# Kernel optimization log

Measured on AMD Instinct MI355X. Metric: run time of the kernel, lower is better.

Reference implementation:

```python
import jax, jax.numpy as jnp
import numpy as np

N = 50000
E = 800000
IN_C, HID_C, OUT_C = 128, 128, 40
K = 3  # PyG TAGConv default number of hops


def setup_inputs() -> dict:
    key = jax.random.key(0)
    k1, k2, k3, k4, k5, k6, k7 = jax.random.split(key, 7)
    x = jax.random.normal(k1, (N, IN_C), dtype=jnp.float32)
    edge_index = jax.random.randint(k2, (2, E), 0, N, dtype=jnp.int64)
    # Linear((K+1)*in, out) weights (stored as [in_total, out] for x @ W)
    s1 = 1.0 / np.sqrt((K + 1) * IN_C)
    s2 = 1.0 / np.sqrt((K + 1) * HID_C)
    W1 = jax.random.uniform(k3, ((K + 1) * IN_C, HID_C), jnp.float32, -s1, s1)
    b1 = jax.random.uniform(k4, (HID_C,), jnp.float32, -s1, s1)
    W2 = jax.random.uniform(k5, ((K + 1) * HID_C, OUT_C), jnp.float32, -s2, s2)
    b2 = jax.random.uniform(k6, (OUT_C,), jnp.float32, -s2, s2)
    return {"x": x, "edge_index": edge_index, "W1": W1, "b1": b1, "W2": W2, "b2": b2}


def _sym_norm(src, dst):
    # GCN-style symmetric normalization: deg computed on destination (col)
    deg = jax.ops.segment_sum(jnp.ones((E,), jnp.float32), dst, num_segments=N)
    dis = jnp.where(deg > 0, jax.lax.rsqrt(jnp.maximum(deg, 1.0)), 0.0)
    return dis[src] * dis[dst]  # [E]


def _tag_layer(x, src, dst, norm, W, b):
    xs = [x]
    h = x
    for _ in range(K):
        h = jax.ops.segment_sum(h[src] * norm[:, None], dst, num_segments=N)
        xs.append(h)
    return jnp.concatenate(xs, axis=1) @ W + b


def reference(x, edge_index, W1, b1, W2, b2):
    src, dst = edge_index[0], edge_index[1]
    norm = _sym_norm(src, dst)
    h = jax.nn.relu(_tag_layer(x, src, dst, norm, W1, b1))
    # F.dropout(training=False) is identity at inference
    h = _tag_layer(h, src, dst, norm, W2, b2)
    return jax.nn.log_softmax(h, axis=1)
```

## Files before the change

### kernel.cpp

```cpp
#include <hip/hip_runtime.h>
#include <hip/hip_bf16.h>

#define NNODES 50000
#define NROWP  50176
#define NEDGES 800000
#define KHOP 3
#define NBKT 196
#define BCAP 6144
#define ABLK 800
#define ACH  1000

typedef __attribute__((ext_vector_type(8))) short short8v;
typedef __attribute__((ext_vector_type(8))) __bf16 bf16x8;
typedef __attribute__((ext_vector_type(4))) float f32x4;

__device__ inline unsigned short f2bf(float f) {
  unsigned u = __builtin_bit_cast(unsigned, f);
  u += 0x7fffu + ((u >> 16) & 1u);
  return (unsigned short)(u >> 16);
}
__device__ inline float bflo(unsigned u) { return __builtin_bit_cast(float, u << 16); }
__device__ inline float bfhi(unsigned u) { return __builtin_bit_cast(float, u & 0xffff0000u); }

__device__ inline void gload_lds16(const void* g, void* l) {
  __builtin_amdgcn_global_load_lds(
      (const __attribute__((address_space(1))) unsigned int*)g,
      (__attribute__((address_space(3))) unsigned int*)l, 16, 0, 0);
}

__device__ inline f32x4 mfma_bf16(bf16x8 a, bf16x8 b, f32x4 c) {
  return __builtin_amdgcn_mfma_f32_16x16x32_bf16(a, b, c, 0, 0, 0);
}

__device__ inline void fma8(float* acc, float w, short8v v) {
  uint4 u = __builtin_bit_cast(uint4, v);
  acc[0] = fmaf(w, bflo(u.x), acc[0]);
  acc[1] = fmaf(w, bfhi(u.x), acc[1]);
  acc[2] = fmaf(w, bflo(u.y), acc[2]);
  acc[3] = fmaf(w, bfhi(u.y), acc[3]);
  acc[4] = fmaf(w, bflo(u.z), acc[4]);
  acc[5] = fmaf(w, bfhi(u.z), acc[5]);
  acc[6] = fmaf(w, bflo(u.w), acc[6]);
  acc[7] = fmaf(w, bfhi(u.w), acc[7]);
}

__device__ inline void fma4(float* acc, float w, uint2 v) {
  acc[0] = fmaf(w, bflo(v.x), acc[0]);
  acc[1] = fmaf(w, bfhi(v.x), acc[1]);
  acc[2] = fmaf(w, bflo(v.y), acc[2]);
  acc[3] = fmaf(w, bfhi(v.y), acc[3]);
}

__global__ __launch_bounds__(256) void bucketA_kernel(
    const int* __restrict__ src, const int* __restrict__ dst,
    int* __restrict__ bcur, int2* __restrict__ bkt) {
  __shared__ int2 eb[ACH];
  __shared__ int hist[256];
  __shared__ int base[256];
  int tid = threadIdx.x;
  int e0 = blockIdx.x * ACH;
  int cnt = NEDGES - e0; if (cnt > ACH) cnt = ACH;
  hist[tid] = 0;
  __syncthreads();
  for (int i = tid; i < cnt; i += 256) {
    int s = src[e0 + i], d = dst[e0 + i];
    eb[i] = make_int2(s, d);
    atomicAdd(&hist[d >> 8], 1);
  }
  __syncthreads();
  base[tid] = atomicAdd(&bcur[tid], hist[tid]);
  hist[tid] = 0;
  __syncthreads();
  for (int i = tid; i < cnt; i += 256) {
    int2 e = eb[i];
    int b = e.y >> 8;
    int off = atomicAdd(&hist[b], 1);
    bkt[(size_t)b * BCAP + base[b] + off] = e;
  }
}

__global__ __launch_bounds__(256) void bktscan_kernel(
    const int* __restrict__ bcur, int* __restrict__ boff, int* __restrict__ row_ptr) {
  __shared__ int sd[256];
  int tid = threadIdx.x;
  int own = (tid < NBKT) ? bcur[tid] : 0;
  sd[tid] = own;
  __syncthreads();
  for (int o = 1; o < 256; o <<= 1) {
    int t = (tid >= o) ? sd[tid - o] : 0;
    __syncthreads();
    sd[tid] += t;
    __syncthreads();
  }
  if (tid < NBKT) boff[tid] = sd[tid] - own;
  if (tid == 255) row_ptr[NNODES] = sd[255];
}

__global__ __launch_bounds__(256) void histC_kernel(
    const int* __restrict__ bcur, const int2* __restrict__ bkt,
    const int* __restrict__ boff, int* __restrict__ row_ptr,
    float* __restrict__ dis, int n) {
  __shared__ int h[256];
  __shared__ int sc[256];
  int b = blockIdx.x, tid = threadIdx.x;
  h[tid] = 0;
  __syncthreads();
  int sz = bcur[b];
  for (int i = tid; i < sz; i += 256)
    atomicAdd(&h[bkt[(size_t)b * BCAP + i].y & 255], 1);
  __syncthreads();
  int own = h[tid];
  sc[tid] = own;
  __syncthreads();
  for (int o = 1; o < 256; o <<= 1) {
    int t = (tid >= o) ? sc[tid - o] : 0;
    __syncthreads();
    sc[tid] += t;
    __syncthreads();
  }
  int node = b * 256 + tid;
  if (node < n) {
    row_ptr[node] = boff[b] + sc[tid] - own;
    dis[node] = (own > 0) ? rsqrtf((float)own) : 0.f;
  }
}

__global__ __launch_bounds__(256) void scatB_kernel(
    const int* __restrict__ bcur, const int2* __restrict__ bkt,
    const int* __restrict__ row_ptr, const float* __restrict__ dis,
    int2* __restrict__ csr, int n) {
  __shared__ int cur[256];
  int b = blockIdx.x, tid = threadIdx.x;
  int node = b * 256 + tid;
  cur[tid] = (node < n) ? row_ptr[node] : 0;
  __syncthreads();
  int sz = bcur[b];
  for (int i = tid; i < sz; i += 256) {
    int2 e = bkt[(size_t)b * BCAP + i];
    int pos = atomicAdd(&cur[e.y & 255], 1);
    int2 ent;
    ent.x = e.x;
    ent.y = __float_as_int(dis[e.x] * dis[e.y]);
    csr[pos] = ent;
  }
}

__global__ void wprep_kernel(const float* __restrict__ W1, const float* __restrict__ W2,
                             unsigned short* __restrict__ W1t,
                             unsigned short* __restrict__ W2pt) {
  int t = blockIdx.x * blockDim.x + threadIdx.x;
  if (t < 512 * 128) {
    int c = t >> 9, k = t & 511;
    W1t[t] = f2bf(W1[(size_t)k * 128 + c]);
  } else if (t < 512 * 128 + 160 * 128) {
    int u = t - 512 * 128;
    int q = u >> 7, r = u & 127;
    int k = q / 40, c = q - k * 40;
    W2pt[u] = f2bf(W2[(size_t)(k * 128 + r) * 40 + c]);
  }
}

__global__ void copyx_kernel(const float* __restrict__ x, unsigned short* __restrict__ P, int n) {
  int t = blockIdx.x * blockDim.x + threadIdx.x;
  int i = t >> 5;
  int c4 = (t & 31) << 2;
  if (i < n) {
    float4 v = *(const float4*)&x[(size_t)i * 128 + c4];
    unsigned lo = (unsigned)f2bf(v.x) | ((unsigned)f2bf(v.y) << 16);
    unsigned hi = (unsigned)f2bf(v.z) | ((unsigned)f2bf(v.w) << 16);
    uint2 o; o.x = lo; o.y = hi;
    *(uint2*)&P[(size_t)i * 512 + c4] = o;
  }
}

__global__ __launch_bounds__(256) void prop128c_kernel(
    const unsigned short* __restrict__ in, unsigned short* __restrict__ out,
    const int* __restrict__ row_ptr, const int2* __restrict__ csr, int n) {
  int node = (int)((blockIdx.x * blockDim.x + threadIdx.x) >> 6);
  int lane = threadIdx.x & 63;
  if (node >= n) return;
  int beg = row_ptr[node], end = row_ptr[node + 1];
  int deg = end - beg;
  int2 ent = make_int2(0, 0);
  if (lane < deg) ent = csr[beg + lane];
  const int grp = lane >> 4, sub = lane & 15;
  float acc[8] = {0.f, 0.f, 0.f, 0.f, 0.f, 0.f, 0.f, 0.f};
  int m = deg < 64 ? deg : 64;
  int j = 0;
  for (; j + 16 <= m; j += 16) {
    int s0 = __shfl(ent.x, j + grp, 64);
    float w0 = __int_as_float(__shfl(ent.y, j + grp, 64));
    int s1 = __shfl(ent.x, j + 4 + grp, 64);
    float w1 = __int_as_float(__shfl(ent.y, j + 4 + grp, 64));
    int s2 = __shfl(ent.x, j + 8 + grp, 64);
    float w2 = __int_as_float(__shfl(ent.y, j + 8 + grp, 64));
    int s3 = __shfl(ent.x, j + 12 + grp, 64);
    float w3 = __int_as_float(__shfl(ent.y, j + 12 + grp, 64));
    short8v v0 = *(const short8v*)(in + (size_t)s0 * 512 + sub * 8);
    short8v v1 = *(const short8v*)(in + (size_t)s1 * 512 + sub * 8);
    short8v v2 = *(const short8v*)(in + (size_t)s2 * 512 + sub * 8);
    short8v v3 = *(const short8v*)(in + (size_t)s3 * 512 + sub * 8);
    fma8(acc, w0, v0);
    fma8(acc, w1, v1);
    fma8(acc, w2, v2);
    fma8(acc, w3, v3);
  }
  for (; j + 8 <= m; j += 8) {
    int s0 = __shfl(ent.x, j + grp, 64);
    float w0 = __int_as_float(__shfl(ent.y, j + grp, 64));
    int s1 = __shfl(ent.x, j + 4 + grp, 64);
    float w1 = __int_as_float(__shfl(ent.y, j + 4 + grp, 64));
    short8v v0 = *(const short8v*)(in + (size_t)s0 * 512 + sub * 8);
    short8v v1 = *(const short8v*)(in + (size_t)s1 * 512 + sub * 8);
    fma8(acc, w0, v0);
    fma8(acc, w1, v1);
  }
  for (; j < m; j += 4) {
    int idx = j + grp;
    bool act = idx < m;
    int ic = act ? idx : m - 1;
    int s0 = __shfl(ent.x, ic, 64);
    float w0 = __int_as_float(__shfl(ent.y, ic, 64));
    if (!act) w0 = 0.f;
    short8v v0 = *(const short8v*)(in + (size_t)s0 * 512 + sub * 8);
    fma8(acc, w0, v0);
  }
  for (int t = beg + 64; t < end; ++t) {
    int2 e0 = csr[t];
    float w0 = (grp == 0) ? __int_as_float(e0.y) : 0.f;
    short8v v = *(const short8v*)(in + (size_t)e0.x * 512 + sub * 8);
    fma8(acc, w0, v);
  }
#pragma unroll
  for (int i = 0; i < 8; ++i) {
    acc[i] += __shfl_xor(acc[i], 16, 64);
    acc[i] += __shfl_xor(acc[i], 32, 64);
  }
  if (grp == 0) {
    uint4 r;
    r.x = (unsigned)f2bf(acc[0]) | ((unsigned)f2bf(acc[1]) << 16);
    r.y = (unsigned)f2bf(acc[2]) | ((unsigned)f2bf(acc[3]) << 16);
    r.z = (unsigned)f2bf(acc[4]) | ((unsigned)f2bf(acc[5]) << 16);
    r.w = (unsigned)f2bf(acc[6]) | ((unsigned)f2bf(acc[7]) << 16);
    *(uint4*)(out + (size_t)node * 512 + sub * 8) = r;
  }
}

__global__ __launch_bounds__(256) void gemm12_kernel(
    const unsigned short* __restrict__ A,
    const unsigned short* __restrict__ B1t,
    const float* __restrict__ bias,
    const unsigned short* __restrict__ B2t,
    unsigned short* __restrict__ G) {
  __shared__ short smem[2048 + 4096 + 64 * 136];
  short* As  = smem;
  short* Bs1 = smem + 2048;
  short* Ht  = smem + 2048 + 4096;
  short* Bs2c = smem;
  const int tid = threadIdx.x;
  const int lane = tid & 63;
  const int w = tid >> 6;
  const int wr = w & 1;
  const int wc = w >> 1;
  const int row0 = blockIdx.x * 64;
  const int lrow = lane >> 2;
  const int lkp = lane & 3;
  const int kg = lane >> 4, rr = lane & 15;

  f32x4 acc[2][4];
#pragma unroll
  for (int i = 0; i < 2; ++i)
#pragma unroll
    for (int j = 0; j < 4; ++j) acc[i][j] = (f32x4)0.f;

  for (int k0 = 0; k0 < 512; k0 += 32) {
    gload_lds16(A + (size_t)(row0 + w * 16 + lrow) * 512 + k0 + lkp * 8, &As[w * 512]);
    gload_lds16(B1t + (size_t)(w * 16 + lrow) * 512 + k0 + lkp * 8, &Bs1[w * 512]);
    gload_lds16(B1t + (size_t)((w + 4) * 16 + lrow) * 512 + k0 + lkp * 8, &Bs1[(w + 4) * 512]);
    __syncthreads();
    bf16x8 af[2], bfr[4];
#pragma unroll
    for (int mr = 0; mr < 2; ++mr)
      af[mr] = __builtin_bit_cast(bf16x8,
          *(const short8v*)&As[(wr * 32 + mr * 16 + rr) * 32 + kg * 8]);
#pragma unroll
    for (int nr = 0; nr < 4; ++nr)
      bfr[nr] = __builtin_bit_cast(bf16x8,
          *(const short8v*)&Bs1[(wc * 64 + nr * 16 + rr) * 32 + kg * 8]);
#pragma unroll
    for (int mr = 0; mr < 2; ++mr)
#pragma unroll
      for (int nr = 0; nr < 4; ++nr)
        acc[mr][nr] = mfma_bf16(af[mr], bfr[nr], acc[mr][nr]);
    __syncthreads();
  }
  {
    const int cg = lane >> 4, cl = lane & 15;
#pragma unroll
    for (int mr = 0; mr < 2; ++mr)
#pragma unroll
      for (int nr = 0; nr < 4; ++nr) {
        int col = wc * 64 + nr * 16 + cl;
        float bv = bias[col];
#pragma unroll
        for (int j = 0; j < 4; ++j) {
          int lr = wr * 32 + mr * 16 + cg * 4 + j;
          Ht[lr * 136 + col] = (short)f2bf(fmaxf(acc[mr][nr][j] + bv, 0.f));
        }
      }
  }
  __syncthreads();

  f32x4 acc2[10];
#pragma unroll
  for (int i = 0; i < 10; ++i) acc2[i] = (f32x4)0.f;

  for (int k0 = 0; k0 < 128; k0 += 32) {
    for (int c = w; c < 10; c += 4)
      gload_lds16(B2t + (size_t)(c * 16 + lrow) * 128 + k0 + lkp * 8, &Bs2c[c * 512]);
    __syncthreads();
    bf16x8 af = __builtin_bit_cast(bf16x8,
        *(const short8v*)&Ht[(w * 16 + rr) * 136 + k0 + kg * 8]);
#pragma unroll
    for (int nr = 0; nr < 10; ++nr) {
      bf16x8 bfr = __builtin_bit_cast(bf16x8,
          *(const short8v*)&Bs2c[(nr * 16 + rr) * 32 + kg * 8]);
      acc2[nr] = mfma_bf16(af, bfr, acc2[nr]);
    }
    __syncthreads();
  }
  {
    const int cg = lane >> 4, cl = lane & 15;
#pragma unroll
    for (int nr = 0; nr < 10; ++nr) {
      int col = nr * 16 + cl;
      int k = col / 40;
      int o = col - k * 40;
#pragma unroll
      for (int j = 0; j < 4; ++j) {
        int row = row0 + w * 16 + cg * 4 + j;
        G[(size_t)k * NROWP * 64 + (size_t)row * 64 + o] = f2bf(acc2[nr][j]);
      }
    }
  }
}

__global__ __launch_bounds__(256) void prop40c_kernel(
    const unsigned short* __restrict__ in,
    const unsigned short* __restrict__ add,
    unsigned short* __restrict__ out,
    const int* __restrict__ row_ptr, const int2* __restrict__ csr, int n) {
  int node = (int)((blockIdx.x * blockDim.x + threadIdx.x) >> 6);
  int lane = threadIdx.x & 63;
  if (node >= n) return;
  int beg = row_ptr[node], end = row_ptr[node + 1];
  int deg = end - beg;
  int2 ent = make_int2(0, 0);
  if (lane < deg) ent = csr[beg + lane];
  const int grp = lane >> 4, sub = lane & 15;
  float acc[4] = {0.f, 0.f, 0.f, 0.f};
  if (grp == 0) {
    uint2 a = *(const uint2*)(add + (size_t)node * 64 + sub * 4);
    acc[0] = bflo(a.x); acc[1] = bfhi(a.x);
    acc[2] = bflo(a.y); acc[3] = bfhi(a.y);
  }
  int m = deg < 64 ? deg : 64;
  int j = 0;
  for (; j + 16 <= m; j += 16) {
    int s0 = __shfl(ent.x, j + grp, 64);
    float w0 = __int_as_float(__shfl(ent.y, j + grp, 64));
    int s1 = __shfl(ent.x, j + 4 + grp, 64);
    float w1 = __int_as_float(__shfl(ent.y, j + 4 + grp, 64));
    int s2 = __shfl(ent.x, j + 8 + grp, 64);
    float w2 = __int_as_float(__shfl(ent.y, j + 8 + grp, 64));
    int s3 = __shfl(ent.x, j + 12 + grp, 64);
    float w3 = __int_as_float(__shfl(ent.y, j + 12 + grp, 64));
    uint2 v0 = *(const uint2*)(in + (size_t)s0 * 64 + sub * 4);
    uint2 v1 = *(const uint2*)(in + (size_t)s1 * 64 + sub * 4);
    uint2 v2 = *(const uint2*)(in + (size_t)s2 * 64 + sub * 4);
    uint2 v3 = *(const uint2*)(in + (size_t)s3 * 64 + sub * 4);
    fma4(acc, w0, v0);
    fma4(acc, w1, v1);
    fma4(acc, w2, v2);
    fma4(acc, w3, v3);
  }
  for (; j + 8 <= m; j += 8) {
    int s0 = __shfl(ent.x, j + grp, 64);
    float w0 = __int_as_float(__shfl(ent.y, j + grp, 64));
    int s1 = __shfl(ent.x, j + 4 + grp, 64);
    float w1 = __int_as_float(__shfl(ent.y, j + 4 + grp, 64));
    uint2 v0 = *(const uint2*)(in + (size_t)s0 * 64 + sub * 4);
    uint2 v1 = *(const uint2*)(in + (size_t)s1 * 64 + sub * 4);
    fma4(acc, w0, v0);
    fma4(acc, w1, v1);
  }
  for (; j < m; j += 4) {
    int idx = j + grp;
    bool act = idx < m;
    int ic = act ? idx : m - 1;
    int s0 = __shfl(ent.x, ic, 64);
    float w0 = __int_as_float(__shfl(ent.y, ic, 64));
    if (!act) w0 = 0.f;
    uint2 v0 = *(const uint2*)(in + (size_t)s0 * 64 + sub * 4);
    fma4(acc, w0, v0);
  }
  for (int t = beg + 64; t < end; ++t) {
    int2 e0 = csr[t];
    float w = (grp == 0) ? __int_as_float(e0.y) : 0.f;
    uint2 v = *(const uint2*)(in + (size_t)e0.x * 64 + sub * 4);
    fma4(acc, w, v);
  }
#pragma unroll
  for (int i = 0; i < 4; ++i) {
    acc[i] += __shfl_xor(acc[i], 16, 64);
    acc[i] += __shfl_xor(acc[i], 32, 64);
  }
  if (grp == 0) {
    uint2 r;
    r.x = (unsigned)f2bf(acc[0]) | ((unsigned)f2bf(acc[1]) << 16);
    r.y = (unsigned)f2bf(acc[2]) | ((unsigned)f2bf(acc[3]) << 16);
    *(uint2*)(out + (size_t)node * 64 + sub * 4) = r;
  }
}

__global__ __launch_bounds__(256) void prop40c_lsm_kernel(
    const unsigned short* __restrict__ in,
    const unsigned short* __restrict__ add,
    const float* __restrict__ b2,
    float* __restrict__ out,
    const int* __restrict__ row_ptr, const int2* __restrict__ csr, int n) {
  int node = (int)((blockIdx.x * blockDim.x + threadIdx.x) >> 6);
  int lane = threadIdx.x & 63;
  if (node >= n) return;
  int beg = row_ptr[node], end = row_ptr[node + 1];
  int deg = end - beg;
  int2 ent = make_int2(0, 0);
  if (lane < deg) ent = csr[beg + lane];
  const int grp = lane >> 4, sub = lane & 15;
  float acc[4] = {0.f, 0.f, 0.f, 0.f};
  if (grp == 0) {
    uint2 a = *(const uint2*)(add + (size_t)node * 64 + sub * 4);
    acc[0] = bflo(a.x); acc[1] = bfhi(a.x);
    acc[2] = bflo(a.y); acc[3] = bfhi(a.y);
  }
  int m = deg < 64 ? deg : 64;
  int j = 0;
  for (; j + 16 <= m; j += 16) {
    int s0 = __shfl(ent.x, j + grp, 64);
    float w0 = __int_as_float(__shfl(ent.y, j + grp, 64));
    int s1 = __shfl(ent.x, j + 4 + grp, 64);
    float w1 = __int_as_float(__shfl(ent.y, j + 4 + grp, 64));
    int s2 = __shfl(ent.x, j + 8 + grp, 64);
    float w2 = __int_as_float(__shfl(ent.y, j + 8 + grp, 64));
    int s3 = __shfl(ent.x, j + 12 + grp, 64);
    float w3 = __int_as_float(__shfl(ent.y, j + 12 + grp, 64));
    uint2 v0 = *(const uint2*)(in + (size_t)s0 * 64 + sub * 4);
    uint2 v1 = *(const uint2*)(in + (size_t)s1 * 64 + sub * 4);
    uint2 v2 = *(const uint2*)(in + (size_t)s2 * 64 + sub * 4);
    uint2 v3 = *(const uint2*)(in + (size_t)s3 * 64 + sub * 4);
    fma4(acc, w0, v0);
    fma4(acc, w1, v1);
    fma4(acc, w2, v2);
    fma4(acc, w3, v3);
  }
  for (; j + 8 <= m; j += 8) {
    int s0 = __shfl(ent.x, j + grp, 64);
    float w0 = __int_as_float(__shfl(ent.y, j + grp, 64));
    int s1 = __shfl(ent.x, j + 4 + grp, 64);
    float w1 = __int_as_float(__shfl(ent.y, j + 4 + grp, 64));
    uint2 v0 = *(const uint2*)(in + (size_t)s0 * 64 + sub * 4);
    uint2 v1 = *(const uint2*)(in + (size_t)s1 * 64 + sub * 4);
    fma4(acc, w0, v0);
    fma4(acc, w1, v1);
  }
  for (; j < m; j += 4) {
    int idx = j + grp;
    bool act = idx < m;
    int ic = act ? idx : m - 1;
    int s0 = __shfl(ent.x, ic, 64);
    float w0 = __int_as_float(__shfl(ent.y, ic, 64));
    if (!act) w0 = 0.f;
    uint2 v0 = *(const uint2*)(in + (size_t)s0 * 64 + sub * 4);
    fma4(acc, w0, v0);
  }
  for (int t = beg + 64; t < end; ++t) {
    int2 e0 = csr[t];
    float w = (grp == 0) ? __int_as_float(e0.y) : 0.f;
    uint2 v = *(const uint2*)(in + (size_t)e0.x * 64 + sub * 4);
    fma4(acc, w, v);
  }
#pragma unroll
  for (int i = 0; i < 4; ++i) {
    acc[i] += __shfl_xor(acc[i], 16, 64);
    acc[i] += __shfl_xor(acc[i], 32, 64);
  }
  bool val = (sub < 10);
  float vv[4];
  if (val) {
    float4 bv = *(const float4*)(b2 + sub * 4);
    vv[0] = acc[0] + bv.x; vv[1] = acc[1] + bv.y;
    vv[2] = acc[2] + bv.z; vv[3] = acc[3] + bv.w;
  } else {
    vv[0] = vv[1] = vv[2] = vv[3] = -__builtin_inff();
  }
  float mx = fmaxf(fmaxf(vv[0], vv[1]), fmaxf(vv[2], vv[3]));
#pragma unroll
  for (int o = 1; o < 16; o <<= 1) mx = fmaxf(mx, __shfl_xor(mx, o, 64));
  float s = 0.f;
  if (val)
    s = expf(vv[0] - mx) + expf(vv[1] - mx) + expf(vv[2] - mx) + expf(vv[3] - mx);
#pragma unroll
  for (int o = 1; o < 16; o <<= 1) s += __shfl_xor(s, o, 64);
  if (grp == 0 && val) {
    float ls = logf(s);
    float4 o4;
    o4.x = vv[0] - mx - ls; o4.y = vv[1] - mx - ls;
    o4.z = vv[2] - mx - ls; o4.w = vv[3] - mx - ls;
    *(float4*)(out + (size_t)node * 40 + sub * 4) = o4;
  }
}

extern "C" void kernel_launch(void* const* d_in, const int* in_sizes, int n_in,
                              void* d_out, int out_size, void* d_ws, size_t ws_size,
                              hipStream_t stream) {
  const float* x  = (const float*)d_in[0];
  const int*   ei = (const int*)d_in[1];
  const float* W1 = (const float*)d_in[2];
  const float* b1 = (const float*)d_in[3];
  const float* W2 = (const float*)d_in[4];
  const float* b2 = (const float*)d_in[5];
  const int* srcv = ei;
  const int* dstv = ei + NEDGES;
  float* out = (float*)d_out;

  char* wsb = (char*)d_ws;
  size_t off = 0;
  auto alloc = [&](size_t bytes) {
    char* p = wsb + off;
    off += (bytes + 255) & ~(size_t)255;
    return p;
  };
  float*          dis     = (float*)          alloc((size_t)NNODES * 4);
  int*            row_ptr = (int*)            alloc(((size_t)NNODES + 1) * 4);
  int*            bcur    = (int*)            alloc((size_t)256 * 4);
  int*            boff    = (int*)            alloc((size_t)NBKT * 4);
  int2*           bkt     = (int2*)           alloc((size_t)NBKT * BCAP * 8);
  int2*           csr     = (int2*)           alloc((size_t)NEDGES * 8);
  unsigned short* W1t     = (unsigned short*) alloc((size_t)128 * 512 * 2);
  unsigned short* W2pt    = (unsigned short*) alloc((size_t)160 * 128 * 2);
  unsigned short* P       = (unsigned short*) alloc((size_t)NROWP * 512 * 2);
  unsigned short* G       = (unsigned short*) alloc((size_t)4 * NROWP * 64 * 2);
  unsigned short* tb      = (unsigned short*) alloc((size_t)NNODES * 64 * 2);
  unsigned short* t2      = (unsigned short*) alloc((size_t)NNODES * 64 * 2);

  unsigned short* G0 = G;
  unsigned short* G1 = G + (size_t)1 * NROWP * 64;
  unsigned short* G2 = G + (size_t)2 * NROWP * 64;
  unsigned short* G3 = G + (size_t)3 * NROWP * 64;

  hipMemsetAsync(bcur, 0, 256 * 4, stream);
  bucketA_kernel<<<ABLK, 256, 0, stream>>>(srcv, dstv, bcur, bkt);
  bktscan_kernel<<<1, 256, 0, stream>>>(bcur, boff, row_ptr);
  histC_kernel<<<NBKT, 256, 0, stream>>>(bcur, bkt, boff, row_ptr, dis, NNODES);
  scatB_kernel<<<NBKT, 256, 0, stream>>>(bcur, bkt, row_ptr, dis, csr, NNODES);
  wprep_kernel<<<(512 * 128 + 160 * 128 + 255) / 256, 256, 0, stream>>>(W1, W2, W1t, W2pt);
  copyx_kernel<<<((NNODES * 32) + 255) / 256, 256, 0, stream>>>(x, P, NNODES);

  const int prop_blocks = (NNODES * 64 + 255) / 256;
  for (int k = 1; k <= KHOP; ++k)
    prop128c_kernel<<<prop_blocks, 256, 0, stream>>>(P + 128 * (k - 1), P + 128 * k,
                                                     row_ptr, csr, NNODES);
  const int gemm_blocks = (NNODES + 63) / 64;
  gemm12_kernel<<<gemm_blocks, 256, 0, stream>>>(P, W1t, b1, W2pt, G);
  prop40c_kernel<<<prop_blocks, 256, 0, stream>>>(G3, G2, tb, row_ptr, csr, NNODES);
  prop40c_kernel<<<prop_blocks, 256, 0, stream>>>(tb, G1, t2, row_ptr, csr, NNODES);
  prop40c_lsm_kernel<<<prop_blocks, 256, 0, stream>>>(t2, G0, b2, out, row_ptr, csr, NNODES);
}
```

Measured before the change: 229.6 us.

## Merge scan into histC, fuse prep kernels, widen prop40 to 8-lane groups

Folds the single-block bucket scan into every histC block, which recomputes the prefix redundantly, and merges the x-to-bf16 copy with the weight prep into one kernel, cutting the launch count. The 40-wide propagation kernels now have each lane load 16 bytes (8 bf16) instead of 8. Each row is then covered by 8 lanes rather than 16, so 8 edges are processed per step instead of 4. This trades more registers and shuffle-reduction steps for fewer, wider memory transactions.

```diff
diff --git a/kernel.cpp b/kernel.cpp
--- a/kernel.cpp
+++ b/kernel.cpp
@@ -44,13 +44,6 @@
   acc[7] = fmaf(w, bfhi(u.w), acc[7]);
 }
 
-__device__ inline void fma4(float* acc, float w, uint2 v) {
-  acc[0] = fmaf(w, bflo(v.x), acc[0]);
-  acc[1] = fmaf(w, bfhi(v.x), acc[1]);
-  acc[2] = fmaf(w, bflo(v.y), acc[2]);
-  acc[3] = fmaf(w, bfhi(v.y), acc[3]);
-}
-
 __global__ __launch_bounds__(256) void bucketA_kernel(
     const int* __restrict__ src, const int* __restrict__ dst,
     int* __restrict__ bcur, int2* __restrict__ bkt) {
@@ -79,32 +72,23 @@
   }
 }
 
-__global__ __launch_bounds__(256) void bktscan_kernel(
-    const int* __restrict__ bcur, int* __restrict__ boff, int* __restrict__ row_ptr) {
-  __shared__ int sd[256];
-  int tid = threadIdx.x;
-  int own = (tid < NBKT) ? bcur[tid] : 0;
-  sd[tid] = own;
-  __syncthreads();
-  for (int o = 1; o < 256; o <<= 1) {
-    int t = (tid >= o) ? sd[tid - o] : 0;
-    __syncthreads();
-    sd[tid] += t;
-    __syncthreads();
-  }
-  if (tid < NBKT) boff[tid] = sd[tid] - own;
-  if (tid == 255) row_ptr[NNODES] = sd[255];
-}
-
 __global__ __launch_bounds__(256) void histC_kernel(
     const int* __restrict__ bcur, const int2* __restrict__ bkt,
-    const int* __restrict__ boff, int* __restrict__ row_ptr,
-    float* __restrict__ dis, int n) {
+    int* __restrict__ row_ptr, float* __restrict__ dis, int n) {
   __shared__ int h[256];
   __shared__ int sc[256];
+  __shared__ int bo[256];
   int b = blockIdx.x, tid = threadIdx.x;
   h[tid] = 0;
-  __syncthreads();
+  bo[tid] = (tid < NBKT) ? bcur[tid] : 0;
+  __syncthreads();
+  for (int o = 1; o < 256; o <<= 1) {
+    int t = (tid >= o) ? bo[tid - o] : 0;
+    __syncthreads();
+    bo[tid] += t;
+    __syncthreads();
+  }
+  if (b == 0 && tid == 255) row_ptr[NNODES] = bo[255];
   int sz = bcur[b];
   for (int i = tid; i < sz; i += 256)
     atomicAdd(&h[bkt[(size_t)b * BCAP + i].y & 255], 1);
@@ -120,7 +104,7 @@
   }
   int node = b * 256 + tid;
   if (node < n) {
-    row_ptr[node] = boff[b] + sc[tid] - own;
+    row_ptr[node] = (bo[b] - sz) + sc[tid] - own;
     dis[node] = (own > 0) ? rsqrtf((float)own) : 0.f;
   }
 }
@@ -145,31 +129,30 @@
   }
 }
 
-__global__ void wprep_kernel(const float* __restrict__ W1, const float* __restrict__ W2,
-                             unsigned short* __restrict__ W1t,
-                             unsigned short* __restrict__ W2pt) {
+__global__ void prep_kernel(const float* __restrict__ x, const float* __restrict__ W1,
+                            const float* __restrict__ W2,
+                            unsigned short* __restrict__ P,
+                            unsigned short* __restrict__ W1t,
+                            unsigned short* __restrict__ W2pt, int n) {
   int t = blockIdx.x * blockDim.x + threadIdx.x;
-  if (t < 512 * 128) {
-    int c = t >> 9, k = t & 511;
-    W1t[t] = f2bf(W1[(size_t)k * 128 + c]);
-  } else if (t < 512 * 128 + 160 * 128) {
-    int u = t - 512 * 128;
-    int q = u >> 7, r = u & 127;
-    int k = q / 40, c = q - k * 40;
-    W2pt[u] = f2bf(W2[(size_t)(k * 128 + r) * 40 + c]);
-  }
-}
-
-__global__ void copyx_kernel(const float* __restrict__ x, unsigned short* __restrict__ P, int n) {
-  int t = blockIdx.x * blockDim.x + threadIdx.x;
-  int i = t >> 5;
-  int c4 = (t & 31) << 2;
-  if (i < n) {
+  const int NC = NNODES * 32;
+  if (t < NC) {
+    int i = t >> 5;
+    int c4 = (t & 31) << 2;
     float4 v = *(const float4*)&x[(size_t)i * 128 + c4];
     unsigned lo = (unsigned)f2bf(v.x) | ((unsigned)f2bf(v.y) << 16);
     unsigned hi = (unsigned)f2bf(v.z) | ((unsigned)f2bf(v.w) << 16);
     uint2 o; o.x = lo; o.y = hi;
     *(uint2*)&P[(size_t)i * 512 + c4] = o;
+  } else if (t < NC + 512 * 128) {
+    int u = t - NC;
+    int c = u >> 9, k = u & 511;
+    W1t[u] = f2bf(W1[(size_t)k * 128 + c]);
+  } else if (t < NC + 512 * 128 + 160 * 128) {
+    int u = t - NC - 512 * 128;
+    int q = u >> 7, r = u & 127;
+    int k = q / 40, c = q - k * 40;
+    W2pt[u] = f2bf(W2[(size_t)(k * 128 + r) * 40 + c]);
   }
 }
 
@@ -345,7 +328,7 @@
   }
 }
 
-__global__ __launch_bounds__(256) void prop40c_kernel(
+__global__ __launch_bounds__(256) void prop40e_kernel(
     const unsigned short* __restrict__ in,
     const unsigned short* __restrict__ add,
     unsigned short* __restrict__ out,
@@ -357,73 +340,57 @@
   int deg = end - beg;
   int2 ent = make_int2(0, 0);
   if (lane < deg) ent = csr[beg + lane];
-  const int grp = lane >> 4, sub = lane & 15;
-  float acc[4] = {0.f, 0.f, 0.f, 0.f};
+  const int grp = lane >> 3, sub = lane & 7;
+  float acc[8] = {0.f, 0.f, 0.f, 0.f, 0.f, 0.f, 0.f, 0.f};
   if (grp == 0) {
-    uint2 a = *(const uint2*)(add + (size_t)node * 64 + sub * 4);
-    acc[0] = bflo(a.x); acc[1] = bfhi(a.x);
-    acc[2] = bflo(a.y); acc[3] = bfhi(a.y);
+    short8v a = *(const short8v*)(add + (size_t)node * 64 + sub * 8);
+    fma8(acc, 1.0f, a);
   }
   int m = deg < 64 ? deg : 64;
   int j = 0;
   for (; j + 16 <= m; j += 16) {
     int s0 = __shfl(ent.x, j + grp, 64);
     float w0 = __int_as_float(__shfl(ent.y, j + grp, 64));
-    int s1 = __shfl(ent.x, j + 4 + grp, 64);
-    float w1 = __int_as_float(__shfl(ent.y, j + 4 + grp, 64));
-    int s2 = __shfl(ent.x, j + 8 + grp, 64);
-    float w2 = __int_as_float(__shfl(ent.y, j + 8 + grp, 64));
-    int s3 = __shfl(ent.x, j + 12 + grp, 64);
-    float w3 = __int_as_float(__shfl(ent.y, j + 12 + grp, 64));
-    uint2 v0 = *(const uint2*)(in + (size_t)s0 * 64 + sub * 4);
-    uint2 v1 = *(const uint2*)(in + (size_t)s1 * 64 + sub * 4);
-    uint2 v2 = *(const uint2*)(in + (size_t)s2 * 64 + sub * 4);
-    uint2 v3 = *(const uint2*)(in + (size_t)s3 * 64 + sub * 4);
-    fma4(acc, w0, v0);
-    fma4(acc, w1, v1);
-    fma4(acc, w2, v2);
-    fma4(acc, w3, v3);
-  }
-  for (; j + 8 <= m; j += 8) {
-    int s0 = __shfl(ent.x, j + grp, 64);
-    float w0 = __int_as_float(__shfl(ent.y, j + grp, 64));
-    int s1 = __shfl(ent.x, j + 4 + grp, 64);
-    float w1 = __int_as_float(__shfl(ent.y, j + 4 + grp, 64));
-    uint2 v0 = *(const uint2*)(in + (size_t)s0 * 64 + sub * 4);
-    uint2 v1 = *(const uint2*)(in + (size_t)s1 * 64 + sub * 4);
-    fma4(acc, w0, v0);
-    fma4(acc, w1, v1);
-  }
-  for (; j < m; j += 4) {
+    int s1 = __shfl(ent.x, j + 8 + grp, 64);
+    float w1 = __int_as_float(__shfl(ent.y, j + 8 + grp, 64));
+    short8v v0 = *(const short8v*)(in + (size_t)s0 * 64 + sub * 8);
+    short8v v1 = *(const short8v*)(in + (size_t)s1 * 64 + sub * 8);
+    fma8(acc, w0, v0);
+    fma8(acc, w1, v1);
+  }
+  for (; j < m; j += 8) {
     int idx = j + grp;
     bool act = idx < m;
     int ic = act ? idx : m - 1;
     int s0 = __shfl(ent.x, ic, 64);
     float w0 = __int_as_float(__shfl(ent.y, ic, 64));
     if (!act) w0 = 0.f;
-    uint2 v0 = *(const uint2*)(in + (size_t)s0 * 64 + sub * 4);
-    fma4(acc, w0, v0);
+    short8v v0 = *(const short8v*)(in + (size_t)s0 * 64 + sub * 8);
+    fma8(acc, w0, v0);
   }
   for (int t = beg + 64; t < end; ++t) {
     int2 e0 = csr[t];
     float w = (grp == 0) ? __int_as_float(e0.y) : 0.f;
-    uint2 v = *(const uint2*)(in + (size_t)e0.x * 64 + sub * 4);
-    fma4(acc, w, v);
-  }
-#pragma unroll
-  for (int i = 0; i < 4; ++i) {
+    short8v v = *(const short8v*)(in + (size_t)e0.x * 64 + sub * 8);
+    fma8(acc, w, v);
+  }
+#pragma unroll
+  for (int i = 0; i < 8; ++i) {
+    acc[i] += __shfl_xor(acc[i], 8, 64);
     acc[i] += __shfl_xor(acc[i], 16, 64);
     acc[i] += __shfl_xor(acc[i], 32, 64);
   }
   if (grp == 0) {
-    uint2 r;
+    uint4 r;
     r.x = (unsigned)f2bf(acc[0]) | ((unsigned)f2bf(acc[1]) << 16);
     r.y = (unsigned)f2bf(acc[2]) | ((unsigned)f2bf(acc[3]) << 16);
-    *(uint2*)(out + (size_t)node * 64 + sub * 4) = r;
-  }
-}
-
-__global__ __launch_bounds__(256) void prop40c_lsm_kernel(
+    r.z = (unsigned)f2bf(acc[4]) | ((unsigned)f2bf(acc[5]) << 16);
+    r.w = (unsigned)f2bf(acc[6]) | ((unsigned)f2bf(acc[7]) << 16);
+    *(uint4*)(out + (size_t)node * 64 + sub * 8) = r;
+  }
+}
+
+__global__ __launch_bounds__(256) void prop40e_lsm_kernel(
     const unsigned short* __restrict__ in,
     const unsigned short* __restrict__ add,
     const float* __restrict__ b2,
@@ -436,87 +403,80 @@
   int deg = end - beg;
   int2 ent = make_int2(0, 0);
   if (lane < deg) ent = csr[beg + lane];
-  const int grp = lane >> 4, sub = lane & 15;
-  float acc[4] = {0.f, 0.f, 0.f, 0.f};
+  const int grp = lane >> 3, sub = lane & 7;
+  float acc[8] = {0.f, 0.f, 0.f, 0.f, 0.f, 0.f, 0.f, 0.f};
   if (grp == 0) {
-    uint2 a = *(const uint2*)(add + (size_t)node * 64 + sub * 4);
-    acc[0] = bflo(a.x); acc[1] = bfhi(a.x);
-    acc[2] = bflo(a.y); acc[3] = bfhi(a.y);
+    short8v a = *(const short8v*)(add + (size_t)node * 64 + sub * 8);
+    fma8(acc, 1.0f, a);
   }
   int m = deg < 64 ? deg : 64;
   int j = 0;
   for (; j + 16 <= m; j += 16) {
     int s0 = __shfl(ent.x, j + grp, 64);
     float w0 = __int_as_float(__shfl(ent.y, j + grp, 64));
-    int s1 = __shfl(ent.x, j + 4 + grp, 64);
-    float w1 = __int_as_float(__shfl(ent.y, j + 4 + grp, 64));
-    int s2 = __shfl(ent.x, j + 8 + grp, 64);
-    float w2 = __int_as_float(__shfl(ent.y, j + 8 + grp, 64));
-    int s3 = __shfl(ent.x, j + 12 + grp, 64);
-    float w3 = __int_as_float(__shfl(ent.y, j + 12 + grp, 64));
-    uint2 v0 = *(const uint2*)(in + (size_t)s0 * 64 + sub * 4);
-    uint2 v1 = *(const uint2*)(in + (size_t)s1 * 64 + sub * 4);
-    uint2 v2 = *(const uint2*)(in + (size_t)s2 * 64 + sub * 4);
-    uint2 v3 = *(const uint2*)(in + (size_t)s3 * 64 + sub * 4);
-    fma4(acc, w0, v0);
-    fma4(acc, w1, v1);
-    fma4(acc, w2, v2);
-    fma4(acc, w3, v3);
-  }
-  for (; j + 8 <= m; j += 8) {
-    int s0 = __shfl(ent.x, j + grp, 64);
-    float w0 = __int_as_float(__shfl(ent.y, j + grp, 64));
-    int s1 = __shfl(ent.x, j + 4 + grp, 64);
-    float w1 = __int_as_float(__shfl(ent.y, j + 4 + grp, 64));
-    uint2 v0 = *(const uint2*)(in + (size_t)s0 * 64 + sub * 4);
-    uint2 v1 = *(const uint2*)(in + (size_t)s1 * 64 + sub * 4);
-    fma4(acc, w0, v0);
-    fma4(acc, w1, v1);
-  }
-  for (; j < m; j += 4) {
+    int s1 = __shfl(ent.x, j + 8 + grp, 64);
+    float w1 = __int_as_float(__shfl(ent.y, j + 8 + grp, 64));
+    short8v v0 = *(const short8v*)(in + (size_t)s0 * 64 + sub * 8);
+    short8v v1 = *(const short8v*)(in + (size_t)s1 * 64 + sub * 8);
+    fma8(acc, w0, v0);
+    fma8(acc, w1, v1);
+  }
+  for (; j < m; j += 8) {
     int idx = j + grp;
     bool act = idx < m;
     int ic = act ? idx : m - 1;
     int s0 = __shfl(ent.x, ic, 64);
     float w0 = __int_as_float(__shfl(ent.y, ic, 64));
     if (!act) w0 = 0.f;
-    uint2 v0 = *(const uint2*)(in + (size_t)s0 * 64 + sub * 4);
-    fma4(acc, w0, v0);
+    short8v v0 = *(const short8v*)(in + (size_t)s0 * 64 + sub * 8);
+    fma8(acc, w0, v0);
   }
   for (int t = beg + 64; t < end; ++t) {
     int2 e0 = csr[t];
     float w = (grp == 0) ? __int_as_float(e0.y) : 0.f;
-    uint2 v = *(const uint2*)(in + (size_t)e0.x * 64 + sub * 4);
-    fma4(acc, w, v);
-  }
-#pragma unroll
-  for (int i = 0; i < 4; ++i) {
+    short8v v = *(const short8v*)(in + (size_t)e0.x * 64 + sub * 8);
+    fma8(acc, w, v);
+  }
+#pragma unroll
+  for (int i = 0; i < 8; ++i) {
+    acc[i] += __shfl_xor(acc[i], 8, 64);
     acc[i] += __shfl_xor(acc[i], 16, 64);
     acc[i] += __shfl_xor(acc[i], 32, 64);
   }
-  bool val = (sub < 10);
-  float vv[4];
+  bool val = (sub < 5);
+  float vv[8];
   if (val) {
-    float4 bv = *(const float4*)(b2 + sub * 4);
-    vv[0] = acc[0] + bv.x; vv[1] = acc[1] + bv.y;
-    vv[2] = acc[2] + bv.z; vv[3] = acc[3] + bv.w;
+    float4 b0 = *(const float4*)(b2 + sub * 8);
+    float4 b1v = *(const float4*)(b2 + sub * 8 + 4);
+    vv[0] = acc[0] + b0.x; vv[1] = acc[1] + b0.y;
+    vv[2] = acc[2] + b0.z; vv[3] = acc[3] + b0.w;
+    vv[4] = acc[4] + b1v.x; vv[5] = acc[5] + b1v.y;
+    vv[6] = acc[6] + b1v.z; vv[7] = acc[7] + b1v.w;
   } else {
-    vv[0] = vv[1] = vv[2] = vv[3] = -__builtin_inff();
-  }
-  float mx = fmaxf(fmaxf(vv[0], vv[1]), fmaxf(vv[2], vv[3]));
-#pragma unroll
-  for (int o = 1; o < 16; o <<= 1) mx = fmaxf(mx, __shfl_xor(mx, o, 64));
+#pragma unroll
+    for (int i = 0; i < 8; ++i) vv[i] = -__builtin_inff();
+  }
+  float mx = vv[0];
+#pragma unroll
+  for (int i = 1; i < 8; ++i) mx = fmaxf(mx, vv[i]);
+#pragma unroll
+  for (int o = 1; o < 8; o <<= 1) mx = fmaxf(mx, __shfl_xor(mx, o, 64));
   float s = 0.f;
-  if (val)
-    s = expf(vv[0] - mx) + expf(vv[1] - mx) + expf(vv[2] - mx) + expf(vv[3] - mx);
-#pragma unroll
-  for (int o = 1; o < 16; o <<= 1) s += __shfl_xor(s, o, 64);
+  if (val) {
+#pragma unroll
+    for (int i = 0; i < 8; ++i) s += expf(vv[i] - mx);
+  }
+#pragma unroll
+  for (int o = 1; o < 8; o <<= 1) s += __shfl_xor(s, o, 64);
   if (grp == 0 && val) {
     float ls = logf(s);
-    float4 o4;
-    o4.x = vv[0] - mx - ls; o4.y = vv[1] - mx - ls;
-    o4.z = vv[2] - mx - ls; o4.w = vv[3] - mx - ls;
-    *(float4*)(out + (size_t)node * 40 + sub * 4) = o4;
+    float4 o0, o1;
+    o0.x = vv[0] - mx - ls; o0.y = vv[1] - mx - ls;
+    o0.z = vv[2] - mx - ls; o0.w = vv[3] - mx - ls;
+    o1.x = vv[4] - mx - ls; o1.y = vv[5] - mx - ls;
+    o1.z = vv[6] - mx - ls; o1.w = vv[7] - mx - ls;
+    *(float4*)(out + (size_t)node * 40 + sub * 8) = o0;
+    *(float4*)(out + (size_t)node * 40 + sub * 8 + 4) = o1;
   }
 }
 
@@ -543,7 +503,6 @@
   float*          dis     = (float*)          alloc((size_t)NNODES * 4);
   int*            row_ptr = (int*)            alloc(((size_t)NNODES + 1) * 4);
   int*            bcur    = (int*)            alloc((size_t)256 * 4);
-  int*            boff    = (int*)            alloc((size_t)NBKT * 4);
   int2*           bkt     = (int2*)           alloc((size_t)NBKT * BCAP * 8);
   int2*           csr     = (int2*)           alloc((size_t)NEDGES * 8);
   unsigned short* W1t     = (unsigned short*) alloc((size_t)128 * 512 * 2);
@@ -560,11 +519,10 @@
 
   hipMemsetAsync(bcur, 0, 256 * 4, stream);
   bucketA_kernel<<<ABLK, 256, 0, stream>>>(srcv, dstv, bcur, bkt);
-  bktscan_kernel<<<1, 256, 0, stream>>>(bcur, boff, row_ptr);
-  histC_kernel<<<NBKT, 256, 0, stream>>>(bcur, bkt, boff, row_ptr, dis, NNODES);
+  histC_kernel<<<NBKT, 256, 0, stream>>>(bcur, bkt, row_ptr, dis, NNODES);
   scatB_kernel<<<NBKT, 256, 0, stream>>>(bcur, bkt, row_ptr, dis, csr, NNODES);
-  wprep_kernel<<<(512 * 128 + 160 * 128 + 255) / 256, 256, 0, stream>>>(W1, W2, W1t, W2pt);
-  copyx_kernel<<<((NNODES * 32) + 255) / 256, 256, 0, stream>>>(x, P, NNODES);
+  const int prep_threads = NNODES * 32 + 512 * 128 + 160 * 128;
+  prep_kernel<<<(prep_threads + 255) / 256, 256, 0, stream>>>(x, W1, W2, P, W1t, W2pt, NNODES);
 
   const int prop_blocks = (NNODES * 64 + 255) / 256;
   for (int k = 1; k <= KHOP; ++k)
@@ -572,7 +530,7 @@
                                                      row_ptr, csr, NNODES);
   const int gemm_blocks = (NNODES + 63) / 64;
   gemm12_kernel<<<gemm_blocks, 256, 0, stream>>>(P, W1t, b1, W2pt, G);
-  prop40c_kernel<<<prop_blocks, 256, 0, stream>>>(G3, G2, tb, row_ptr, csr, NNODES);
-  prop40c_kernel<<<prop_blocks, 256, 0, stream>>>(tb, G1, t2, row_ptr, csr, NNODES);
-  prop40c_lsm_kernel<<<prop_blocks, 256, 0, stream>>>(t2, G0, b2, out, row_ptr, csr, NNODES);
-}
+  prop40e_kernel<<<prop_blocks, 256, 0, stream>>>(G3, G2, tb, row_ptr, csr, NNODES);
+  prop40e_kernel<<<prop_blocks, 256, 0, stream>>>(tb, G1, t2, row_ptr, csr, NNODES);
+  prop40e_lsm_kernel<<<prop_blocks, 256, 0, stream>>>(t2, G0, b2, out, row_ptr, csr, NNODES);
+}
```

New measurement: 232.6 us. Within noise of the previous version (+1.3%).
